# Optimization experiments

Measured on AMD Instinct MI355X. Metric: run time of the kernel, lower is better.

Reference implementation:

```python
import jax, jax.numpy as jnp
import numpy as np

N = 32768       # nodes
IN = 256        # in_channels
D = 128         # out_channels (per-head dim)
H = 4           # num_heads
M = 4           # num_reps (seeds per partition)
KP = 128        # number of partitions
S = N // KP     # partition size (equal-size partitions)
SCALE = float(np.sqrt(D))


def _linear_init(key, fan_in, fan_out):
    # torch nn.Linear default: U(-1/sqrt(fan_in), 1/sqrt(fan_in)) for W and b
    kw, kb = jax.random.split(key)
    bound = 1.0 / np.sqrt(fan_in)
    w = jax.random.uniform(kw, (fan_in, fan_out), jnp.float32, -bound, bound)
    b = jax.random.uniform(kb, (fan_out,), jnp.float32, -bound, bound)
    return w, b


def setup_inputs() -> dict:
    key = jax.random.key(0)
    k0, k1, k2, k3, k4 = jax.random.split(key, 5)
    x = jax.random.normal(k0, (N, IN), jnp.float32)
    # equal-size disjoint partitions: [KP, S] index array covering 0..N-1
    partition_indices = jnp.arange(N, dtype=jnp.int32).reshape(KP, S)
    Wq_w, Wq_b = _linear_init(k1, IN, H * D)
    Wk_w, Wk_b = _linear_init(k2, IN, H * D)
    Wv_w, Wv_b = _linear_init(k3, IN, H * D)
    pool_seeds = jax.random.normal(k4, (M, H, D), jnp.float32) * 0.02
    alpha_logit = jnp.float32(0.0)
    beta = jnp.float32(1.0)
    return {
        "x": x, "partition_indices": partition_indices,
        "Wq_w": Wq_w, "Wq_b": Wq_b, "Wk_w": Wk_w, "Wk_b": Wk_b,
        "Wv_w": Wv_w, "Wv_b": Wv_b, "pool_seeds": pool_seeds,
        "alpha_logit": alpha_logit, "beta": beta,
    }


def reference(x, partition_indices, Wq_w, Wq_b, Wk_w, Wk_b, Wv_w, Wv_b,
              pool_seeds, alpha_logit, beta):
    n = x.shape[0]
    Q = (x @ Wq_w + Wq_b).reshape(n, H, D)
    K = (x @ Wk_w + Wk_b).reshape(n, H, D)
    V = (x @ Wv_w + Wv_b).reshape(n, H, D)

    # gather per partition -> [KP, S, H, D]
    Qp = Q[partition_indices]
    Kp = K[partition_indices]
    Vp = V[partition_indices]

    # Fine: exact softmax attention within each partition
    attn_local = jnp.einsum('kphd,kqhd->khpq', Qp, Kp) / SCALE
    attn_local = jax.nn.softmax(attn_local, axis=-1)
    outp = jnp.einsum('khpq,kqhd->kphd', attn_local, Vp)  # [KP,S,H,D]
    # partitions are disjoint -> scatter-set back to node order
    out_local = jnp.zeros((n, H, D), x.dtype).at[partition_indices.reshape(-1)].set(
        outp.reshape(n, H, D))
    x_local = out_local.mean(axis=1)  # [N, D]

    # Coarse: learned seeds pool each partition
    pool_attn = jnp.einsum('mhd,kqhd->kmhq', pool_seeds, Kp) / SCALE
    pool_attn = jax.nn.softmax(pool_attn, axis=-1)
    reps_k = jnp.einsum('kmhq,kqhd->kmhd', pool_attn, Kp).reshape(KP * M, H, D)
    reps_v = jnp.einsum('kmhq,kqhd->kmhd', pool_attn, Vp).reshape(KP * M, H, D)

    # Global cross-attention: every node attends to all partition reps
    cross_attn = jnp.einsum('nhd,rhd->nhr', Q, reps_k) / SCALE
    cross_attn = jax.nn.softmax(cross_attn, axis=-1)
    out_global = jnp.einsum('nhr,rhd->nhd', cross_attn, reps_v)
    x_global = out_global.mean(axis=1)  # [N, D]

    x_self = V.mean(axis=1)
    alpha = jax.nn.sigmoid(alpha_logit)
    return alpha * x_local + (1.0 - alpha) * x_global + beta * x_self
```

## Files before the change

kernel.cpp:

```cpp
#include <hip/hip_runtime.h>
#include <hip/hip_bf16.h>


#define INV_SCALE 0.08838834764831845f
#define C2EXP 0.12751744f
#define DEFER_THR 90.50966799f

typedef __attribute__((ext_vector_type(8))) short bf16x8;
typedef __attribute__((ext_vector_type(4))) float floatx4;
typedef unsigned short ushort_t;
typedef unsigned int uint32;

#define OFF_Q    0ull
#define OFF_K    33554432ull
#define OFF_V    67108864ull
#define OFF_LOC  100663296ull
#define OFF_RPK  109051904ull
#define OFF_XC   110100480ull
#define OFF_WC   126877696ull
#define OFF_SCAL 127671296ull
#define OFF_FLAG 127671304ull
#define OFF_RVT  127672320ull
#define OFF_GLB  128196608ull

#define WC_WQ 0
#define WC_WK 131072
#define WC_WV 262144
#define WC_BQ 393216
#define WC_BK 393728
#define WC_BV 394240
#define WC_SEED 394752
#define WC_TOT 396800

static __device__ __forceinline__ float bflo(uint32 u) {
  return __uint_as_float(u << 16);
}
static __device__ __forceinline__ float bfhi(uint32 u) {
  return __uint_as_float(u & 0xffff0000u);
}
static __device__ __forceinline__ float bf2f(ushort_t u) {
  return __uint_as_float(((uint32)u) << 16);
}
static __device__ __forceinline__ ushort_t f2bf(float f) {
  uint32 x = __float_as_uint(f);
  uint32 r = x + 0x7fffu + ((x >> 16) & 1u);
  return (ushort_t)(r >> 16);
}
static __device__ __forceinline__ uint32 pack2bf(float a, float b) {
  return (uint32)f2bf(a) | ((uint32)f2bf(b) << 16);
}

static __device__ __forceinline__ void gl2lds16(const ushort_t* g, ushort_t* l) {
  __builtin_amdgcn_global_load_lds(
      (const __attribute__((address_space(1))) void*)g,
      (__attribute__((address_space(3))) void*)l, 16, 0, 0);
}

__global__ __launch_bounds__(64) void k_detect(const uint32* __restrict__ xw,
                                               const ushort_t* __restrict__ betaRaw,
                                               uint32* __restrict__ flags) {
  const int lane = threadIdx.x;
  const uint32 w = xw[lane * 137 + 3];
  const int e = (w >> 7) & 0xff;
  const unsigned long long b = __ballot(e >= 100 && e <= 140);
  if (lane == 0) {
    flags[0] = (__popcll(b) >= 48) ? 1u : 0u;
    flags[1] = (betaRaw[0] != 0) ? 1u : 0u;
  }
}

static __device__ __forceinline__ void conv8(const void* src, long j, int isB,
                                             ushort_t* dst) {
  if (isB) {
    *reinterpret_cast<uint4*>(dst) =
        *reinterpret_cast<const uint4*>(reinterpret_cast<const ushort_t*>(src) + j);
  } else {
    const float* f = reinterpret_cast<const float*>(src) + j;
    const float4 a = *reinterpret_cast<const float4*>(f);
    const float4 b = *reinterpret_cast<const float4*>(f + 4);
    uint4 o;
    o.x = pack2bf(a.x, a.y); o.y = pack2bf(a.z, a.w);
    o.z = pack2bf(b.x, b.y); o.w = pack2bf(b.z, b.w);
    *reinterpret_cast<uint4*>(dst) = o;
  }
}

__global__ __launch_bounds__(256) void k_convert(
    const void* __restrict__ x,
    const void* __restrict__ Wq, const void* __restrict__ bq,
    const void* __restrict__ Wk, const void* __restrict__ bk,
    const void* __restrict__ Wv, const void* __restrict__ bv,
    const void* __restrict__ seeds, const void* __restrict__ alpha,
    const void* __restrict__ beta,
    ushort_t* __restrict__ xc, ushort_t* __restrict__ wc,
    float* __restrict__ scal, const uint32* __restrict__ flags)
{
  const int isB = (int)flags[0];
  const long i8 = ((long)blockIdx.x * 256 + threadIdx.x) * 8;
  if (blockIdx.y == 0) {
    conv8(x, i8, isB, xc + i8);
  } else {
    if (i8 < WC_BQ) {
      const int sel = (int)(i8 >> 17);
      const long local = i8 & 131071;
      const int kk = (int)(local >> 9);
      const int nn = (int)(local & 511);
      const void* src = sel == 0 ? Wq : (sel == 1 ? Wk : Wv);
      ushort_t* dstW = wc + sel * 131072;
#pragma unroll
      for (int j = 0; j < 8; ++j) {
        ushort_t v;
        if (isB) v = reinterpret_cast<const ushort_t*>(src)[local + j];
        else     v = f2bf(reinterpret_cast<const float*>(src)[local + j]);
        dstW[(size_t)(nn + j) * 256 + kk] = v;
      }
    } else if (i8 < WC_TOT) {
      const void* src; long j;
      if (i8 < WC_BK)        { src = bq;    j = i8 - WC_BQ; }
      else if (i8 < WC_BV)   { src = bk;    j = i8 - WC_BK; }
      else if (i8 < WC_SEED) { src = bv;    j = i8 - WC_BV; }
      else                   { src = seeds; j = i8 - WC_SEED; }
      conv8(src, j, isB, wc + i8);
    }
    if (blockIdx.x == 0 && threadIdx.x == 0) {
      const int isBS = (int)flags[1];
      scal[0] = isBS ? bf2f(reinterpret_cast<const ushort_t*>(alpha)[0])
                     : reinterpret_cast<const float*>(alpha)[0];
      scal[1] = isBS ? bf2f(reinterpret_cast<const ushort_t*>(beta)[0])
                     : reinterpret_cast<const float*>(beta)[0];
    }
  }
}

__global__ __launch_bounds__(256) void k_qkv(
    const ushort_t* __restrict__ xc, const ushort_t* __restrict__ wc,
    ushort_t* __restrict__ Qb, ushort_t* __restrict__ Kb, ushort_t* __restrict__ Vb)
{
  const int m0 = blockIdx.x * 64;
  const int tid = threadIdx.x, lane = tid & 63, wv = tid >> 6;
  const int l16 = lane & 15, quad = lane >> 4;

  __shared__ __align__(16) ushort_t Xs[64 * 256];
  __shared__ __align__(16) ushort_t Ws[64 * 256];

#pragma unroll
  for (int i = 0; i < 8; ++i) {
    const int id = tid + 256 * i;
    const int row = id >> 5, c = id & 31;
    uint4 v = *reinterpret_cast<const uint4*>(xc + (size_t)(m0 + row) * 256 + c * 8);
    *reinterpret_cast<uint4*>(&Xs[row * 256 + ((c ^ (row & 7)) << 3)]) = v;
  }

  for (int sel = 0; sel < 3; ++sel) {
    const ushort_t* WT   = wc + sel * 131072;
    const ushort_t* bias = wc + WC_BQ + sel * 512;
    ushort_t* out        = sel == 0 ? Qb : (sel == 1 ? Kb : Vb);
    for (int nc = 0; nc < 8; ++nc) {
      const int n0 = nc * 64;
      __syncthreads();
#pragma unroll
      for (int i = 0; i < 8; ++i) {
        const int id = tid + 256 * i;
        const int row = id >> 5, c = id & 31;
        uint4 v = *reinterpret_cast<const uint4*>(WT + (size_t)(n0 + row) * 256 + c * 8);
        *reinterpret_cast<uint4*>(&Ws[row * 256 + ((c ^ (row & 7)) << 3)]) = v;
      }
      __syncthreads();

      floatx4 acc[4] = {};
      const int arow = wv * 16 + l16;
#pragma unroll
      for (int ks = 0; ks < 8; ++ks) {
        const int ac = ks * 4 + quad;
        bf16x8 a = *reinterpret_cast<const bf16x8*>(&Xs[arow * 256 + ((ac ^ (arow & 7)) << 3)]);
#pragma unroll
        for (int nt = 0; nt < 4; ++nt) {
          const int brow = nt * 16 + l16;
          bf16x8 b = *reinterpret_cast<const bf16x8*>(&Ws[brow * 256 + ((ac ^ (brow & 7)) << 3)]);
          acc[nt] = __builtin_amdgcn_mfma_f32_16x16x32_bf16(a, b, acc[nt], 0, 0, 0);
        }
      }

#pragma unroll
      for (int nt = 0; nt < 4; ++nt) {
        const int col = n0 + nt * 16 + l16;
        const float bf = bf2f(bias[col]);
#pragma unroll
        for (int r = 0; r < 4; ++r) {
          const int row = m0 + wv * 16 + quad * 4 + r;
          out[(size_t)row * 512 + col] = f2bf(acc[nt][r] + bf);
        }
      }
    }
  }
}

__global__ __launch_bounds__(256) void k_pool(
    const ushort_t* __restrict__ Kb, const ushort_t* __restrict__ Vb,
    const int* __restrict__ pidx_all, const ushort_t* __restrict__ wc,
    ushort_t* __restrict__ rpk, ushort_t* __restrict__ rvT)
{
  const int k = blockIdx.x, h = blockIdx.y;
  const int tid = threadIdx.x, lane = tid & 63, wv = tid >> 6;
  const int* pidx = pidx_all + k * 256;

  __shared__ __align__(16) ushort_t SB[128 * 256];
  const uint32* SBU = reinterpret_cast<const uint32*>(SB);

#pragma unroll
  for (int i = 0; i < 16; ++i) {
    const int e8 = tid + 256 * i;
    const int q = e8 >> 4, dc = (e8 & 15) * 8;
    uint4 kv = *reinterpret_cast<const uint4*>(Kb + (size_t)pidx[q] * 512 + h * 128 + dc);
    const ushort_t* ku = reinterpret_cast<const ushort_t*>(&kv);
    const int qp = q >> 1, qb = q & 1;
#pragma unroll
    for (int j = 0; j < 8; ++j) {
      const int d = dc + j;
      SB[d * 256 + (((qp ^ (d & 31)) << 1) | qb)] = ku[j];
    }
  }
  __syncthreads();

  float q00, q01, q10, q11;
  {
    const uint32* ssrc = reinterpret_cast<const uint32*>(wc + WC_SEED + (size_t)(wv * 4 + h) * 128);
    float s00 = 0.f, s01 = 0.f, s10 = 0.f, s11 = 0.f;
#pragma unroll 8
    for (int dc = 0; dc < 64; ++dc) {
      const uint32 qv = ssrc[dc];
      const float a0 = bflo(qv), a1 = bfhi(qv);
      const int d0 = dc * 2, d1 = d0 + 1;
      const int c0 = lane ^ (d0 & 31);
      const int c1 = lane ^ (d1 & 31);
      const uint32 u00 = SBU[d0 * 128 + c0];
      const uint32 u01 = SBU[d0 * 128 + c0 + 64];
      const uint32 u10 = SBU[d1 * 128 + c1];
      const uint32 u11 = SBU[d1 * 128 + c1 + 64];
      s00 += a0 * bflo(u00) + a1 * bflo(u10);
      s01 += a0 * bfhi(u00) + a1 * bfhi(u10);
      s10 += a0 * bflo(u01) + a1 * bflo(u11);
      s11 += a0 * bfhi(u01) + a1 * bfhi(u11);
    }
    s00 *= INV_SCALE; s01 *= INV_SCALE; s10 *= INV_SCALE; s11 *= INV_SCALE;
    float mx = fmaxf(fmaxf(s00, s01), fmaxf(s10, s11));
#pragma unroll
    for (int off = 32; off >= 1; off >>= 1) mx = fmaxf(mx, __shfl_xor(mx, off));
    const float e00 = __expf(s00 - mx), e01 = __expf(s01 - mx);
    const float e10 = __expf(s10 - mx), e11 = __expf(s11 - mx);
    float sm = e00 + e01 + e10 + e11;
#pragma unroll
    for (int off = 32; off >= 1; off >>= 1) sm += __shfl_xor(sm, off);
    const float inv = 1.0f / sm;
    q00 = e00 * inv; q01 = e01 * inv; q10 = e10 * inv; q11 = e11 * inv;
  }

  {
    float rk0 = 0.f, rk1 = 0.f;
    const int d0 = 2 * lane, d1 = 2 * lane + 1;
#pragma unroll 4
    for (int qp = 0; qp < 64; ++qp) {
      const float pa = __shfl(q00, qp), pb = __shfl(q01, qp);
      const float pc = __shfl(q10, qp), pd = __shfl(q11, qp);
      const int c0 = qp ^ (d0 & 31);
      const int c1 = qp ^ (d1 & 31);
      const uint32 u0  = SBU[d0 * 128 + c0];
      const uint32 u0b = SBU[d0 * 128 + c0 + 64];
      const uint32 u1  = SBU[d1 * 128 + c1];
      const uint32 u1b = SBU[d1 * 128 + c1 + 64];
      rk0 += pa * bflo(u0) + pb * bfhi(u0) + pc * bflo(u0b) + pd * bfhi(u0b);
      rk1 += pa * bflo(u1) + pb * bfhi(u1) + pc * bflo(u1b) + pd * bfhi(u1b);
    }
    reinterpret_cast<uint32*>(rpk + ((size_t)((k * 4 + wv) * 4 + h)) * 128)[lane] = pack2bf(rk0, rk1);
  }
  __syncthreads();

#pragma unroll
  for (int i = 0; i < 16; ++i) {
    const int e8 = tid + 256 * i;
    const int q = e8 >> 4, dc = (e8 & 15) * 8;
    uint4 vv = *reinterpret_cast<const uint4*>(Vb + (size_t)pidx[q] * 512 + h * 128 + dc);
    *reinterpret_cast<uint4*>(&SB[q * 128 + dc]) = vv;
  }
  __syncthreads();

  {
    float rv0 = 0.f, rv1 = 0.f;
#pragma unroll 4
    for (int qp = 0; qp < 64; ++qp) {
      const float pa = __shfl(q00, qp), pb = __shfl(q01, qp);
      const float pc = __shfl(q10, qp), pd = __shfl(q11, qp);
      const uint32 v00 = SBU[(2 * qp) * 64 + lane];
      const uint32 v01 = SBU[(2 * qp + 1) * 64 + lane];
      const uint32 v10 = SBU[(128 + 2 * qp) * 64 + lane];
      const uint32 v11 = SBU[(129 + 2 * qp) * 64 + lane];
      rv0 += pa * bflo(v00) + pb * bflo(v01) + pc * bflo(v10) + pd * bflo(v11);
      rv1 += pa * bfhi(v00) + pb * bfhi(v01) + pc * bfhi(v10) + pd * bfhi(v11);
    }
    const int rrep = k * 4 + wv;
    rvT[(size_t)(h * 128 + 2 * lane) * 512 + rrep]     = f2bf(rv0);
    rvT[(size_t)(h * 128 + 2 * lane + 1) * 512 + rrep] = f2bf(rv1);
  }
}

__global__ __launch_bounds__(256) void k_fine(
    const ushort_t* __restrict__ Qb, const ushort_t* __restrict__ Kb,
    const ushort_t* __restrict__ Vb, const int* __restrict__ pidx_all,
    ushort_t* __restrict__ locS)
{
  const int k = blockIdx.x, qg = blockIdx.y;
  const int tid = threadIdx.x, lane = tid & 63, wv = tid >> 6;
  const int l16 = lane & 15, quad = lane >> 4;
  const int* pidx = pidx_all + k * 256;

  __shared__ __align__(16) ushort_t Qs[64 * 136];
  __shared__ __align__(16) ushort_t SB2[64 * 136];
  __shared__ __align__(16) ushort_t Ps[4][16 * 72];

  float accS[8][4];
#pragma unroll
  for (int nt = 0; nt < 8; ++nt)
#pragma unroll
    for (int r = 0; r < 4; ++r) accS[nt][r] = 0.f;

  for (int h = 0; h < 4; ++h) {
    __syncthreads();
#pragma unroll
    for (int i = 0; i < 4; ++i) {
      const int e = tid + 256 * i;
      const int r = e >> 4, c8 = (e & 15) * 8;
      uint4 v = *reinterpret_cast<const uint4*>(Qb + (size_t)pidx[qg * 64 + r] * 512 + h * 128 + c8);
      *reinterpret_cast<uint4*>(&Qs[r * 136 + c8]) = v;
    }

    floatx4 O[8] = {};
    float m_i[4], l_i[4];
#pragma unroll
    for (int r = 0; r < 4; ++r) { m_i[r] = -3e38f; l_i[r] = 0.f; }

    for (int c = 0; c < 4; ++c) {
      __syncthreads();
#pragma unroll
      for (int i = 0; i < 4; ++i) {
        const int e = tid + 256 * i;
        const int r = e >> 4, c8 = (e & 15) * 8;
        uint4 v = *reinterpret_cast<const uint4*>(Kb + (size_t)pidx[c * 64 + r] * 512 + h * 128 + c8);
        *reinterpret_cast<uint4*>(&SB2[r * 136 + c8]) = v;
      }
      __syncthreads();

      floatx4 S[4] = {};
#pragma unroll
      for (int ks = 0; ks < 4; ++ks) {
        bf16x8 a = *reinterpret_cast<const bf16x8*>(&Qs[(wv * 16 + l16) * 136 + ks * 32 + quad * 8]);
#pragma unroll
        for (int nt = 0; nt < 4; ++nt) {
          bf16x8 b = *reinterpret_cast<const bf16x8*>(&SB2[(nt * 16 + l16) * 136 + ks * 32 + quad * 8]);
          S[nt] = __builtin_amdgcn_mfma_f32_16x16x32_bf16(a, b, S[nt], 0, 0, 0);
        }
      }
#pragma unroll
      for (int nt = 0; nt < 4; ++nt)
#pragma unroll
        for (int r = 0; r < 4; ++r) S[nt][r] *= INV_SCALE;

#pragma unroll
      for (int r = 0; r < 4; ++r) {
        float cm = fmaxf(fmaxf(S[0][r], S[1][r]), fmaxf(S[2][r], S[3][r]));
#pragma unroll
        for (int off = 1; off <= 8; off <<= 1) cm = fmaxf(cm, __shfl_xor(cm, off));
        const float mn = fmaxf(m_i[r], cm);
        const float sc = __expf(m_i[r] - mn);
        m_i[r] = mn;
        l_i[r] *= sc;
#pragma unroll
        for (int nt = 0; nt < 8; ++nt) O[nt][r] *= sc;
        float ps = 0.f;
#pragma unroll
        for (int nt = 0; nt < 4; ++nt) {
          const float p = __expf(S[nt][r] - mn);
          ps += p;
          Ps[wv][(quad * 4 + r) * 72 + nt * 16 + l16] = f2bf(p);
        }
#pragma unroll
        for (int off = 1; off <= 8; off <<= 1) ps += __shfl_xor(ps, off);
        l_i[r] += ps;
      }
      __syncthreads();

#pragma unroll
      for (int i = 0; i < 4; ++i) {
        const int e = tid + 256 * i;
        const int key = e & 63, dc8 = (e >> 6) * 8;
        uint4 vv = *reinterpret_cast<const uint4*>(Vb + (size_t)pidx[c * 64 + key] * 512 + h * 128 + dc8);
        const ushort_t* u = reinterpret_cast<const ushort_t*>(&vv);
#pragma unroll
        for (int j = 0; j < 8; ++j) {
          const int d = dc8 + j;
          SB2[d * 64 + (((key >> 3) ^ j) << 3) + (key & 7)] = u[j];
        }
      }
      __syncthreads();

#pragma unroll
      for (int ks = 0; ks < 2; ++ks) {
        bf16x8 a = *reinterpret_cast<const bf16x8*>(&Ps[wv][l16 * 72 + ks * 32 + quad * 8]);
#pragma unroll
        for (int nt = 0; nt < 8; ++nt) {
          const int d = nt * 16 + l16;
          const int q8 = ks * 4 + quad;
          bf16x8 b = *reinterpret_cast<const bf16x8*>(&SB2[d * 64 + ((q8 ^ (d & 7)) << 3)]);
          O[nt] = __builtin_amdgcn_mfma_f32_16x16x32_bf16(a, b, O[nt], 0, 0, 0);
        }
      }
    }

#pragma unroll
    for (int r = 0; r < 4; ++r) {
      const float inv = 1.0f / l_i[r];
#pragma unroll
      for (int nt = 0; nt < 8; ++nt) accS[nt][r] += O[nt][r] * inv;
    }
  }

#pragma unroll
  for (int r = 0; r < 4; ++r) {
    const int n = pidx[qg * 64 + wv * 16 + quad * 4 + r];
#pragma unroll
    for (int nt = 0; nt < 8; ++nt)
      locS[(size_t)n * 128 + nt * 16 + l16] = f2bf(accS[nt][r] * 0.25f);
  }
}

__global__ __launch_bounds__(256, 2) void k_cross(
    const ushort_t* __restrict__ Qb, const ushort_t* __restrict__ rpk,
    const ushort_t* __restrict__ rvT, ushort_t* __restrict__ glb)
{
  const int h = blockIdx.y;
  const int n0 = blockIdx.x * 64;
  const int tid = threadIdx.x, lane = tid & 63, wv = tid >> 6;
  const int l16 = lane & 15, quad = lane >> 4;

  __shared__ __align__(16) ushort_t BsK[2][64 * 128];
  __shared__ __align__(16) ushort_t BsV[2][128 * 64];
  __shared__ __align__(16) ushort_t Ps[4][16 * 72];

  bf16x8 qf[4];
  {
    const ushort_t* qrow =
        Qb + (size_t)(n0 + wv * 16 + l16) * 512 + h * 128 + quad * 8;
#pragma unroll
    for (int ks = 0; ks < 4; ++ks)
      qf[ks] = *reinterpret_cast<const bf16x8*>(qrow + ks * 32);
  }

  const int kRL = lane >> 4;
  const int kCH = lane & 15;
  const int vDL = lane >> 3;
  const int vCH = lane & 7;

  floatx4 O[8] = {};
  float m_i = -3e38f, l_i = 0.f;

  {
#pragma unroll
    for (int j = 0; j < 4; ++j) {
      const int row = wv * 16 + j * 4 + kRL;
      gl2lds16(rpk + (size_t)row * 512 + h * 128 + ((kCH ^ (row & 7)) << 3),
               &BsK[0][(wv * 16 + j * 4) * 128]);
      const int d = wv * 32 + j * 8 + vDL;
      gl2lds16(rvT + (size_t)(h * 128 + d) * 512 + ((vCH ^ (d & 7)) << 3),
               &BsV[0][(wv * 32 + j * 8) * 64]);
    }
  }
  __syncthreads();

  const int kswz = l16 & 7;

  for (int c = 0; c < 8; ++c) {
    const int cur = c & 1;

    if (c < 7) {
      const int nb = cur ^ 1;
      const int cn = c + 1;
#pragma unroll
      for (int j = 0; j < 4; ++j) {
        const int row = wv * 16 + j * 4 + kRL;
        gl2lds16(rpk + (size_t)(cn * 64 + row) * 512 + h * 128 +
                     ((kCH ^ (row & 7)) << 3),
                 &BsK[nb][(wv * 16 + j * 4) * 128]);
        const int d = wv * 32 + j * 8 + vDL;
        gl2lds16(rvT + (size_t)(h * 128 + d) * 512 + cn * 64 +
                     ((vCH ^ (d & 7)) << 3),
                 &BsV[nb][(wv * 32 + j * 8) * 64]);
      }
    }

    floatx4 S[4] = {};
#pragma unroll
    for (int ks = 0; ks < 4; ++ks) {
      const int ac = ks * 4 + quad;
#pragma unroll
      for (int nt = 0; nt < 4; ++nt) {
        bf16x8 b = *reinterpret_cast<const bf16x8*>(
            &BsK[cur][(nt * 16 + l16) * 128 + ((ac ^ kswz) << 3)]);
        S[nt] = __builtin_amdgcn_mfma_f32_16x16x32_bf16(b, qf[ks], S[nt], 0, 0, 0);
      }
    }

    float cm;
    {
      const float m0 = fmaxf(fmaxf(S[0][0], S[0][1]), fmaxf(S[0][2], S[0][3]));
      const float m1 = fmaxf(fmaxf(S[1][0], S[1][1]), fmaxf(S[1][2], S[1][3]));
      const float m2 = fmaxf(fmaxf(S[2][0], S[2][1]), fmaxf(S[2][2], S[2][3]));
      const float m3 = fmaxf(fmaxf(S[3][0], S[3][1]), fmaxf(S[3][2], S[3][3]));
      cm = fmaxf(fmaxf(m0, m1), fmaxf(m2, m3));
      cm = fmaxf(cm, __shfl_xor(cm, 16));
      cm = fmaxf(cm, __shfl_xor(cm, 32));
    }
    if (!__all(cm <= m_i + DEFER_THR)) {
      const float mn = fmaxf(m_i, cm);
      const float sc = exp2f((m_i - mn) * C2EXP);
      m_i = mn;
      l_i *= sc;
      float scR[4];
#pragma unroll
      for (int r = 0; r < 4; ++r) scR[r] = __shfl(sc, quad * 4 + r);
#pragma unroll
      for (int nt = 0; nt < 8; ++nt)
#pragma unroll
        for (int r = 0; r < 4; ++r) O[nt][r] *= scR[r];
    }
    {
      const float mC = m_i * C2EXP;
      float ps = 0.f;
#pragma unroll
      for (int nt = 0; nt < 4; ++nt) {
        const float p0 = exp2f(S[nt][0] * C2EXP - mC);
        const float p1 = exp2f(S[nt][1] * C2EXP - mC);
        const float p2 = exp2f(S[nt][2] * C2EXP - mC);
        const float p3 = exp2f(S[nt][3] * C2EXP - mC);
        ps += (p0 + p1) + (p2 + p3);
        uint2 pk2 = make_uint2(pack2bf(p0, p1), pack2bf(p2, p3));
        *reinterpret_cast<uint2*>(&Ps[wv][l16 * 72 + nt * 16 + quad * 4]) = pk2;
      }
      ps += __shfl_xor(ps, 16);
      ps += __shfl_xor(ps, 32);
      l_i += ps;
    }

#pragma unroll
    for (int ks = 0; ks < 2; ++ks) {
      bf16x8 a = *reinterpret_cast<const bf16x8*>(&Ps[wv][l16 * 72 + ks * 32 + quad * 8]);
#pragma unroll
      for (int nt = 0; nt < 8; ++nt) {
        const int q8 = ks * 4 + quad;
        bf16x8 b = *reinterpret_cast<const bf16x8*>(
            &BsV[cur][(nt * 16 + l16) * 64 + ((q8 ^ kswz) << 3)]);
        O[nt] = __builtin_amdgcn_mfma_f32_16x16x32_bf16(a, b, O[nt], 0, 0, 0);
      }
    }

    __syncthreads();
  }

  float invR[4];
#pragma unroll
  for (int r = 0; r < 4; ++r) invR[r] = 1.0f / __shfl(l_i, quad * 4 + r);
#pragma unroll
  for (int r = 0; r < 4; ++r) {
    const int n = n0 + wv * 16 + quad * 4 + r;
#pragma unroll
    for (int nt = 0; nt < 8; ++nt)
      glb[(size_t)n * 512 + h * 128 + nt * 16 + l16] = f2bf(O[nt][r] * invR[r]);
  }
}

__global__ __launch_bounds__(256) void k_combine(
    const ushort_t* __restrict__ locS, const ushort_t* __restrict__ glb,
    const ushort_t* __restrict__ Vb, const float* __restrict__ scal,
    float* __restrict__ out)
{
  const int t = blockIdx.x * 256 + threadIdx.x;
  const int n = t >> 6, dp = t & 63;
  const float alpha = 1.0f / (1.0f + __expf(-scal[0]));
  const float beta = scal[1];
  const uint32 lv = reinterpret_cast<const uint32*>(locS)[(size_t)n * 64 + dp];
  float g0 = 0.f, g1 = 0.f, v0 = 0.f, v1 = 0.f;
#pragma unroll
  for (int hh = 0; hh < 4; ++hh) {
    const uint32 gv = *reinterpret_cast<const uint32*>(glb + (size_t)n * 512 + hh * 128 + 2 * dp);
    const uint32 vv = *reinterpret_cast<const uint32*>(Vb + (size_t)n * 512 + hh * 128 + 2 * dp);
    g0 += bflo(gv); g1 += bfhi(gv);
    v0 += bflo(vv); v1 += bfhi(vv);
  }
  const float r0 = alpha * bflo(lv) + (1.0f - alpha) * g0 * 0.25f + beta * v0 * 0.25f;
  const float r1 = alpha * bfhi(lv) + (1.0f - alpha) * g1 * 0.25f + beta * v1 * 0.25f;
  reinterpret_cast<float2*>(out)[(size_t)n * 64 + dp] = make_float2(r0, r1);
}

extern "C" void kernel_launch(void* const* d_in, const int* in_sizes, int n_in,
                              void* d_out, int out_size, void* d_ws, size_t ws_size,
                              hipStream_t stream) {
  const void* x     = d_in[0];
  const int*  pidx  = (const int*)d_in[1];
  const void* Wq    = d_in[2];
  const void* bq    = d_in[3];
  const void* Wk    = d_in[4];
  const void* bk    = d_in[5];
  const void* Wv    = d_in[6];
  const void* bv    = d_in[7];
  const void* seeds = d_in[8];
  const void* al    = d_in[9];
  const void* be    = d_in[10];

  char* ws = (char*)d_ws;
  ushort_t* Qb   = (ushort_t*)(ws + OFF_Q);
  ushort_t* Kb   = (ushort_t*)(ws + OFF_K);
  ushort_t* Vb   = (ushort_t*)(ws + OFF_V);
  ushort_t* locS = (ushort_t*)(ws + OFF_LOC);
  ushort_t* rpk  = (ushort_t*)(ws + OFF_RPK);
  ushort_t* xc   = (ushort_t*)(ws + OFF_XC);
  ushort_t* wc   = (ushort_t*)(ws + OFF_WC);
  float*    scal = (float*)   (ws + OFF_SCAL);
  uint32*   flags= (uint32*)  (ws + OFF_FLAG);
  ushort_t* rvT  = (ushort_t*)(ws + OFF_RVT);
  ushort_t* glb  = (ushort_t*)(ws + OFF_GLB);

  k_detect<<<1, 64, 0, stream>>>((const uint32*)x, (const ushort_t*)be, flags);
  k_convert<<<dim3(4096, 2), 256, 0, stream>>>(x, Wq, bq, Wk, bk, Wv, bv, seeds, al, be,
                                               xc, wc, scal, flags);
  k_qkv<<<512, 256, 0, stream>>>(xc, wc, Qb, Kb, Vb);
  k_pool<<<dim3(128, 4), 256, 0, stream>>>(Kb, Vb, pidx, wc, rpk, rvT);
  k_fine<<<dim3(128, 4), 256, 0, stream>>>(Qb, Kb, Vb, pidx, locS);
  k_cross<<<dim3(512, 4), 256, 0, stream>>>(Qb, rpk, rvT, glb);
  k_combine<<<8192, 256, 0, stream>>>(locS, glb, Vb, scal, (float*)d_out);
}
```

Before: 366.5 us.

## Double-buffer K tiles via direct global-to-LDS loads and transpose QK in fine attention

Restructures the fine-attention kernel into one flattened loop over heads and key chunks. K tiles are double-buffered with async global-to-LDS loads into a swizzled layout, and Q fragments are held in registers. S is computed transposed so each lane owns one query, and softmax uses exp2 with a folded scale plus a deferred-max rescale that skips O rescaling unless the max grows past a threshold. This aims to hide K load latency, cut LDS traffic and barriers, and reduce per-row shuffle and exp work, at the cost of more registers and a more complex sync pattern.

```diff
diff --git a/kernel.cpp b/kernel.cpp
--- a/kernel.cpp
+++ b/kernel.cpp
@@ -313,114 +313,154 @@
   const int l16 = lane & 15, quad = lane >> 4;
   const int* pidx = pidx_all + k * 256;
 
-  __shared__ __align__(16) ushort_t Qs[64 * 136];
-  __shared__ __align__(16) ushort_t SB2[64 * 136];
+  __shared__ __align__(16) ushort_t BsK[2][64 * 128];
+  __shared__ __align__(16) ushort_t SBV[128 * 64];
   __shared__ __align__(16) ushort_t Ps[4][16 * 72];
 
+  const int qidx = pidx[qg * 64 + wv * 16 + l16];
+
+  const int kRL = lane >> 4;
+  const int kCH = lane & 15;
+  const int kswz = l16 & 7;
+
   float accS[8][4];
 #pragma unroll
   for (int nt = 0; nt < 8; ++nt)
 #pragma unroll
     for (int r = 0; r < 4; ++r) accS[nt][r] = 0.f;
 
-  for (int h = 0; h < 4; ++h) {
+#pragma unroll
+  for (int j = 0; j < 4; ++j) {
+    const int row = wv * 16 + j * 4 + kRL;
+    gl2lds16(Kb + (size_t)pidx[row] * 512 + ((kCH ^ (row & 7)) << 3),
+             &BsK[0][(wv * 16 + j * 4) * 128]);
+  }
+  __syncthreads();
+
+  bf16x8 qf[4];
+  floatx4 O[8];
+  float m_i = -3e38f, l_i = 0.f;
+
+  for (int idx = 0; idx < 16; ++idx) {
+    const int h = idx >> 2, c = idx & 3;
+    const int cur = idx & 1;
+
+    if (c == 0) {
+      const ushort_t* qrow = Qb + (size_t)qidx * 512 + h * 128 + quad * 8;
+#pragma unroll
+      for (int ks = 0; ks < 4; ++ks)
+        qf[ks] = *reinterpret_cast<const bf16x8*>(qrow + ks * 32);
+#pragma unroll
+      for (int nt = 0; nt < 8; ++nt) O[nt] = (floatx4){0.f, 0.f, 0.f, 0.f};
+      m_i = -3e38f;
+      l_i = 0.f;
+    }
+
+    if (idx < 15) {
+      const int hn = (idx + 1) >> 2, cn = (idx + 1) & 3;
+      const int nb = cur ^ 1;
+#pragma unroll
+      for (int j = 0; j < 4; ++j) {
+        const int row = wv * 16 + j * 4 + kRL;
+        gl2lds16(Kb + (size_t)pidx[cn * 64 + row] * 512 + hn * 128 +
+                     ((kCH ^ (row & 7)) << 3),
+                 &BsK[nb][(wv * 16 + j * 4) * 128]);
+      }
+    }
+
+    floatx4 S[4] = {};
+#pragma unroll
+    for (int ks = 0; ks < 4; ++ks) {
+      const int ac = ks * 4 + quad;
+#pragma unroll
+      for (int nt = 0; nt < 4; ++nt) {
+        bf16x8 b = *reinterpret_cast<const bf16x8*>(
+            &BsK[cur][(nt * 16 + l16) * 128 + ((ac ^ kswz) << 3)]);
+        S[nt] = __builtin_amdgcn_mfma_f32_16x16x32_bf16(b, qf[ks], S[nt], 0, 0, 0);
+      }
+    }
+
+    float cm;
+    {
+      const float m0 = fmaxf(fmaxf(S[0][0], S[0][1]), fmaxf(S[0][2], S[0][3]));
+      const float m1 = fmaxf(fmaxf(S[1][0], S[1][1]), fmaxf(S[1][2], S[1][3]));
+      const float m2 = fmaxf(fmaxf(S[2][0], S[2][1]), fmaxf(S[2][2], S[2][3]));
+      const float m3 = fmaxf(fmaxf(S[3][0], S[3][1]), fmaxf(S[3][2], S[3][3]));
+      cm = fmaxf(fmaxf(m0, m1), fmaxf(m2, m3));
+      cm = fmaxf(cm, __shfl_xor(cm, 16));
+      cm = fmaxf(cm, __shfl_xor(cm, 32));
+    }
+    if (!__all(cm <= m_i + DEFER_THR)) {
+      const float mn = fmaxf(m_i, cm);
+      const float sc = exp2f((m_i - mn) * C2EXP);
+      m_i = mn;
+      l_i *= sc;
+      float scR[4];
+#pragma unroll
+      for (int r = 0; r < 4; ++r) scR[r] = __shfl(sc, quad * 4 + r);
+#pragma unroll
+      for (int nt = 0; nt < 8; ++nt)
+#pragma unroll
+        for (int r = 0; r < 4; ++r) O[nt][r] *= scR[r];
+    }
+    {
+      const float mC = m_i * C2EXP;
+      float ps = 0.f;
+#pragma unroll
+      for (int nt = 0; nt < 4; ++nt) {
+        const float p0 = exp2f(S[nt][0] * C2EXP - mC);
+        const float p1 = exp2f(S[nt][1] * C2EXP - mC);
+        const float p2 = exp2f(S[nt][2] * C2EXP - mC);
+        const float p3 = exp2f(S[nt][3] * C2EXP - mC);
+        ps += (p0 + p1) + (p2 + p3);
+        uint2 pk2 = make_uint2(pack2bf(p0, p1), pack2bf(p2, p3));
+        *reinterpret_cast<uint2*>(&Ps[wv][l16 * 72 + nt * 16 + quad * 4]) = pk2;
+      }
+      ps += __shfl_xor(ps, 16);
+      ps += __shfl_xor(ps, 32);
+      l_i += ps;
+    }
+
     __syncthreads();
 #pragma unroll
     for (int i = 0; i < 4; ++i) {
       const int e = tid + 256 * i;
-      const int r = e >> 4, c8 = (e & 15) * 8;
-      uint4 v = *reinterpret_cast<const uint4*>(Qb + (size_t)pidx[qg * 64 + r] * 512 + h * 128 + c8);
-      *reinterpret_cast<uint4*>(&Qs[r * 136 + c8]) = v;
-    }
-
-    floatx4 O[8] = {};
-    float m_i[4], l_i[4];
-#pragma unroll
-    for (int r = 0; r < 4; ++r) { m_i[r] = -3e38f; l_i[r] = 0.f; }
-
-    for (int c = 0; c < 4; ++c) {
-      __syncthreads();
-#pragma unroll
-      for (int i = 0; i < 4; ++i) {
-        const int e = tid + 256 * i;
-        const int r = e >> 4, c8 = (e & 15) * 8;
-        uint4 v = *reinterpret_cast<const uint4*>(Kb + (size_t)pidx[c * 64 + r] * 512 + h * 128 + c8);
-        *reinterpret_cast<uint4*>(&SB2[r * 136 + c8]) = v;
-      }
-      __syncthreads();
-
-      floatx4 S[4] = {};
-#pragma unroll
-      for (int ks = 0; ks < 4; ++ks) {
-        bf16x8 a = *reinterpret_cast<const bf16x8*>(&Qs[(wv * 16 + l16) * 136 + ks * 32 + quad * 8]);
-#pragma unroll
-        for (int nt = 0; nt < 4; ++nt) {
-          bf16x8 b = *reinterpret_cast<const bf16x8*>(&SB2[(nt * 16 + l16) * 136 + ks * 32 + quad * 8]);
-          S[nt] = __builtin_amdgcn_mfma_f32_16x16x32_bf16(a, b, S[nt], 0, 0, 0);
-        }
-      }
-#pragma unroll
-      for (int nt = 0; nt < 4; ++nt)
-#pragma unroll
-        for (int r = 0; r < 4; ++r) S[nt][r] *= INV_SCALE;
-
-#pragma unroll
-      for (int r = 0; r < 4; ++r) {
-        float cm = fmaxf(fmaxf(S[0][r], S[1][r]), fmaxf(S[2][r], S[3][r]));
-#pragma unroll
-        for (int off = 1; off <= 8; off <<= 1) cm = fmaxf(cm, __shfl_xor(cm, off));
-        const float mn = fmaxf(m_i[r], cm);
-        const float sc = __expf(m_i[r] - mn);
-        m_i[r] = mn;
-        l_i[r] *= sc;
-#pragma unroll
-        for (int nt = 0; nt < 8; ++nt) O[nt][r] *= sc;
-        float ps = 0.f;
-#pragma unroll
-        for (int nt = 0; nt < 4; ++nt) {
-          const float p = __expf(S[nt][r] - mn);
-          ps += p;
-          Ps[wv][(quad * 4 + r) * 72 + nt * 16 + l16] = f2bf(p);
-        }
-#pragma unroll
-        for (int off = 1; off <= 8; off <<= 1) ps += __shfl_xor(ps, off);
-        l_i[r] += ps;
-      }
-      __syncthreads();
-
-#pragma unroll
-      for (int i = 0; i < 4; ++i) {
-        const int e = tid + 256 * i;
-        const int key = e & 63, dc8 = (e >> 6) * 8;
-        uint4 vv = *reinterpret_cast<const uint4*>(Vb + (size_t)pidx[c * 64 + key] * 512 + h * 128 + dc8);
-        const ushort_t* u = reinterpret_cast<const ushort_t*>(&vv);
-#pragma unroll
-        for (int j = 0; j < 8; ++j) {
-          const int d = dc8 + j;
-          SB2[d * 64 + (((key >> 3) ^ j) << 3) + (key & 7)] = u[j];
-        }
-      }
-      __syncthreads();
-
-#pragma unroll
-      for (int ks = 0; ks < 2; ++ks) {
-        bf16x8 a = *reinterpret_cast<const bf16x8*>(&Ps[wv][l16 * 72 + ks * 32 + quad * 8]);
-#pragma unroll
-        for (int nt = 0; nt < 8; ++nt) {
-          const int d = nt * 16 + l16;
-          const int q8 = ks * 4 + quad;
-          bf16x8 b = *reinterpret_cast<const bf16x8*>(&SB2[d * 64 + ((q8 ^ (d & 7)) << 3)]);
-          O[nt] = __builtin_amdgcn_mfma_f32_16x16x32_bf16(a, b, O[nt], 0, 0, 0);
-        }
-      }
-    }
-
-#pragma unroll
-    for (int r = 0; r < 4; ++r) {
-      const float inv = 1.0f / l_i[r];
-#pragma unroll
-      for (int nt = 0; nt < 8; ++nt) accS[nt][r] += O[nt][r] * inv;
-    }
+      const int key = e & 63, dc8 = (e >> 6) * 8;
+      uint4 vv = *reinterpret_cast<const uint4*>(
+          Vb + (size_t)pidx[c * 64 + key] * 512 + h * 128 + dc8);
+      const ushort_t* u = reinterpret_cast<const ushort_t*>(&vv);
+#pragma unroll
+      for (int j = 0; j < 8; ++j) {
+        const int d = dc8 + j;
+        SBV[d * 64 + (((key >> 3) ^ j) << 3) + (key & 7)] = u[j];
+      }
+    }
+    __syncthreads();
+
+#pragma unroll
+    for (int ks = 0; ks < 2; ++ks) {
+      bf16x8 a = *reinterpret_cast<const bf16x8*>(&Ps[wv][l16 * 72 + ks * 32 + quad * 8]);
+#pragma unroll
+      for (int nt = 0; nt < 8; ++nt) {
+        const int d = nt * 16 + l16;
+        const int q8 = ks * 4 + quad;
+        bf16x8 b = *reinterpret_cast<const bf16x8*>(
+            &SBV[d * 64 + ((q8 ^ (d & 7)) << 3)]);
+        O[nt] = __builtin_amdgcn_mfma_f32_16x16x32_bf16(a, b, O[nt], 0, 0, 0);
+      }
+    }
+
+    if (c == 3) {
+      float invR[4];
+#pragma unroll
+      for (int r = 0; r < 4; ++r) invR[r] = 1.0f / __shfl(l_i, quad * 4 + r);
+#pragma unroll
+      for (int nt = 0; nt < 8; ++nt)
+#pragma unroll
+        for (int r = 0; r < 4; ++r) accS[nt][r] += O[nt][r] * invR[r];
+    }
+
+    __syncthreads();
   }
 
 #pragma unroll
```

New measurement: 332.1 us. 9.4% less time.
